# Optimization experiments

Measured on AMD Instinct MI355X. Metric: run time of the kernel, lower is better.

## Reference

```python
import jax, jax.numpy as jnp
import numpy as np

B, C, LH, LW, HH, HW = 8, 64, 128, 128, 64, 64


def conv3x3(x, w, groups=1):
    # x: NCHW, w: OIHW, stride 1, padding 1 (matches nn.Conv2d(k=3, p=1, bias=False))
    return jax.lax.conv_general_dilated(
        x, w, window_strides=(1, 1), padding=((1, 1), (1, 1)),
        feature_group_count=groups,
        dimension_numbers=('NCHW', 'OIHW', 'NCHW'))


def grid_sample_bilinear(img, grid):
    # F.grid_sample(mode='bilinear', padding_mode='zeros', align_corners=True)
    # img: (N, Cc, H, W); grid: (N, Ho, Wo, 2) with (x, y) in [-1, 1]
    N, Cc, H, W = img.shape
    gx = (grid[..., 0] + 1.0) * 0.5 * (W - 1)
    gy = (grid[..., 1] + 1.0) * 0.5 * (H - 1)
    x0 = jnp.floor(gx)
    y0 = jnp.floor(gy)
    wx1 = gx - x0
    wy1 = gy - y0

    def tap(xi, yi, wgt):
        valid = (xi >= 0) & (xi <= W - 1) & (yi >= 0) & (yi <= H - 1)
        xc = jnp.clip(xi, 0, W - 1).astype(jnp.int32)
        yc = jnp.clip(yi, 0, H - 1).astype(jnp.int32)
        v = jax.vmap(lambda im, y, x: im[:, y, x])(img, yc, xc)  # (N, Cc, Ho, Wo)
        return v * (wgt * valid)[:, None]

    return (tap(x0, y0, (1 - wx1) * (1 - wy1))
            + tap(x0 + 1, y0, wx1 * (1 - wy1))
            + tap(x0, y0 + 1, (1 - wx1) * wy1)
            + tap(x0 + 1, y0 + 1, wx1 * wy1))


def flow_warp(inp, flow, out_h, out_w):
    # base grid in [-1,1] (align_corners=True convention), flow normalized by (out_w, out_h)
    hs = jnp.linspace(-1.0, 1.0, out_h)
    ws = jnp.linspace(-1.0, 1.0, out_w)
    base = jnp.stack(jnp.meshgrid(ws, hs, indexing='xy'), axis=-1)  # (Ho, Wo, 2) as (x, y)
    norm = jnp.array([out_w, out_h], dtype=inp.dtype)
    grid = base[None].astype(inp.dtype) + jnp.transpose(flow, (0, 2, 3, 1)) / norm
    return grid_sample_bilinear(inp, grid)


def setup_inputs() -> dict:
    key = jax.random.key(0)
    k1, k2, k3, k4, k5, k6 = jax.random.split(key, 6)
    return {
        'low_feature': jax.random.normal(k1, (B, C, LH, LW), dtype=jnp.float32),
        'high_feature': jax.random.normal(k2, (B, C, HH, HW), dtype=jnp.float32),
        'w_conv_l': jax.random.normal(k3, (C, 1, 3, 3), dtype=jnp.float32) * 0.1,   # depthwise
        'w_conv_h': jax.random.normal(k4, (C, 1, 3, 3), dtype=jnp.float32) * 0.1,   # depthwise
        'w_flow': jax.random.normal(k5, (4 * C, C, 3, 3), dtype=jnp.float32) * 0.05,
        'w_gate': jax.random.normal(k6, (1, 4, 3, 3), dtype=jnp.float32) * 0.1,
    }


def reference(low_feature, high_feature, w_conv_l, w_conv_h, w_flow, w_gate):
    lb, ln, lh, lw = low_feature.shape
    hb, hn, hh, hw = high_feature.shape
    l_feature = conv3x3(low_feature, w_conv_l, groups=ln)
    h_feature = conv3x3(high_feature, w_conv_h, groups=hn)
    # F.interpolate(mode='bilinear', align_corners=False) == jax.image.resize bilinear
    h_feature = jax.image.resize(h_feature, (hb, hn, lh, lw), method='bilinear')
    flow = conv3x3(l_feature + h_feature, w_flow)          # (B, 4C, lh, lw)
    part = 2 * ln
    flow_h, flow_l = flow[:, :part], flow[:, part:]
    high_r = high_feature.reshape(hb * hn, 1, hh, hw)
    fh = flow_h.reshape(lb * ln, 2, lh, lw)
    high_warp = flow_warp(high_r, fh, lh, lw).reshape(lb, ln, lh, lw)
    low_r = low_feature.reshape(lb * ln, 1, lh, lw)
    fl = flow_l.reshape(lb * ln, 2, lh, lw)
    low_warp = flow_warp(low_r, fl, lh, lw).reshape(lb, ln, lh, lw)
    gate_in = jnp.concatenate([
        h_feature.mean(axis=1, keepdims=True),
        l_feature.mean(axis=1, keepdims=True),
        h_feature.max(axis=1, keepdims=True),
        l_feature.max(axis=1, keepdims=True)], axis=1)     # (B, 4, lh, lw)
    gates = jax.nn.sigmoid(conv3x3(gate_in, w_gate))
    return high_warp * gates + low_warp * (1.0 - gates)
```

## Files before the change

### kernel.cpp

```cpp
#include <hip/hip_runtime.h>
#include <math.h>

#define BB 8
#define CC 64
#define LHH 128
#define LWW 128
#define HHH 64
#define HWW 64

typedef __attribute__((ext_vector_type(8))) short short8v;
typedef __attribute__((ext_vector_type(4))) float f32x4;

typedef struct __attribute__((packed, aligned(4))) {
  float x, y;
} f2u;

#define BTS 584
#define SROWB 16640
#define SIMGB (130 * SROWB)
#define KROWB 8448

__device__ __forceinline__ unsigned short f2bf(float f) {
  unsigned u = __float_as_uint(f);
  unsigned r = (u + 0x7fffu + ((u >> 16) & 1u)) >> 16;
  return (unsigned short)r;
}

__global__ __launch_bounds__(256) void dw_high_prep_kernel(
    const float* __restrict__ hf, const float* __restrict__ w,
    float* __restrict__ out, const float* __restrict__ wflow,
    unsigned short* __restrict__ bt) {
  if (blockIdx.x >= 8192) {
    int t = (blockIdx.x - 8192) * 256 + threadIdx.x;
    if (t >= 256 * BTS) return;
    int oc2 = t / BTS;
    int kd = t - oc2 * BTS;
    unsigned short v = 0;
    if (kd < 576) {
      int c = oc2 >> 2;
      int j = oc2 & 3;
      int orig = (j >> 1) * 128 + 2 * c + (j & 1);
      int dydx = kd >> 6;
      int ci = kd & 63;
      v = f2bf(wflow[(orig * 64 + ci) * 9 + dydx]);
    }
    bt[t] = v;
    return;
  }
  int t = blockIdx.x * 256 + threadIdx.x;
  int x = t & 63;
  int y = (t >> 6) & 63;
  int c = (t >> 12) & 63;
  int b = t >> 18;
  const float* img = hf + ((size_t)(b * CC + c)) * (HHH * HWW);
  const float* wc = w + c * 9;
  const int xm = max(x - 1, 0), xp = min(x + 1, 63);
  const int ym = max(y - 1, 0), yp = min(y + 1, 63);
  const float mL = x > 0 ? 1.f : 0.f, mR = x < 63 ? 1.f : 0.f;
  const float mT = y > 0 ? 1.f : 0.f, mB = y < 63 ? 1.f : 0.f;
  const bool xz = (x == 0);
  const int dxp = xp - xm;
  f2u p0 = *(const f2u*)(img + ym * 64 + xm);
  f2u p1 = *(const f2u*)(img + y * 64 + xm);
  f2u p2 = *(const f2u*)(img + yp * 64 + xm);
  float r0p = img[ym * 64 + xm + dxp];
  float r1p = img[y * 64 + xm + dxp];
  float r2p = img[yp * 64 + xm + dxp];
  float r0x = xz ? p0.x : p0.y;
  float r1x = xz ? p1.x : p1.y;
  float r2x = xz ? p2.x : p2.y;
  float t0 = (wc[0] * mL) * p0.x + wc[1] * r0x + (wc[2] * mR) * r0p;
  float t1 = (wc[3] * mL) * p1.x + wc[4] * r1x + (wc[5] * mR) * r1p;
  float t2 = (wc[6] * mL) * p2.x + wc[7] * r2x + (wc[8] * mR) * r2p;
  out[t] = mT * t0 + t1 + mB * t2;
}

__global__ __launch_bounds__(512, 4) void fuse_sum_stats_kernel(
    const float* __restrict__ low, const float* __restrict__ hsm,
    const float* __restrict__ wl, unsigned short* __restrict__ sump,
    float* __restrict__ gate_in) {
  __shared__ unsigned short sumS[128 * 64];
  __shared__ float sh[4][4][128];
  __shared__ float wS[576];

  const int bid = blockIdx.x;
  const int b = bid & 7;
  const int y = bid >> 3;
  const int tid = threadIdx.x;
  const int x = tid & 127;
  const int q = tid >> 7;
  char* sbase = (char*)sump + (size_t)b * SIMGB;

  wS[tid] = wl[tid];
  if (tid < 64) wS[512 + tid] = wl[512 + tid];

  {
    const short8v z = {0, 0, 0, 0, 0, 0, 0, 0};
    if (y == 0) {
      for (int i = tid; i < 2080; i += 512) {
        int row = (i < 1040) ? 0 : 129;
        int o = (i % 1040) * 16;
        *(short8v*)(sbase + (size_t)row * SROWB + o) = z;
      }
    }
    if (tid < 16) {
      int side = tid >> 3;
      int o = (tid & 7) * 16;
      *(short8v*)(sbase + (size_t)(y + 1) * SROWB + side * (129 * 128) + o) = z;
    }
  }
  __syncthreads();

  float sy = 0.5f * y - 0.25f;
  float sx = 0.5f * x - 0.25f;
  float y0f = floorf(sy), x0f = floorf(sx);
  float wy = sy - y0f, wx = sx - x0f;
  int iy0 = (int)y0f, ix0 = (int)x0f;
  int iy0c = max(0, min(HHH - 1, iy0));
  int iy1c = max(0, min(HHH - 1, iy0 + 1));
  float w00 = (1.f - wy) * (1.f - wx), w01 = (1.f - wy) * wx;
  float w10 = wy * (1.f - wx), w11 = wy * wx;
  const int hxb = min(max(ix0, 0), HWW - 2);
  const bool hs0 = (ix0 <= hxb);
  const bool hs1 = (ix0 + 1 <= hxb);

  const int xm = max(x - 1, 0), xp = min(x + 1, 127);
  const int ym = max(y - 1, 0), yp = min(y + 1, 127);
  const float mL = x > 0 ? 1.f : 0.f, mR = x < 127 ? 1.f : 0.f;
  const float mT = y > 0 ? 1.f : 0.f, mB = y < 127 ? 1.f : 0.f;
  const bool xz = (x == 0);

  const unsigned lco = (unsigned)((b * CC + q * 16) * 16384);
  const unsigned hco = (unsigned)((b * CC + q * 16) * 4096);
  const unsigned ro0 = (unsigned)(ym * 128 + xm);
  const unsigned ro1 = (unsigned)(y * 128 + xm);
  const unsigned ro2 = (unsigned)(yp * 128 + xm);
  const unsigned dxp = (unsigned)(xp - xm);
  const unsigned ho0 = (unsigned)(iy0c * 64 + hxb);
  const unsigned ho1 = (unsigned)(iy1c * 64 + hxb);

  float hmean = 0.f, lmean = 0.f;
  float hmax = -3.402823466e+38f, lmax = -3.402823466e+38f;

  unsigned short sv[16];
#pragma unroll 8
  for (int j = 0; j < 16; ++j) {
    const unsigned lo_ = lco + (unsigned)(j * 16384);
    const float* wc = &wS[(q * 16 + j) * 9];
    f2u p0 = *(const f2u*)(low + (lo_ + ro0));
    f2u p1 = *(const f2u*)(low + (lo_ + ro1));
    f2u p2 = *(const f2u*)(low + (lo_ + ro2));
    float r0p = low[lo_ + ro0 + dxp];
    float r1p = low[lo_ + ro1 + dxp];
    float r2p = low[lo_ + ro2 + dxp];
    const unsigned ho_ = hco + (unsigned)(j * 4096);
    f2u q0 = *(const f2u*)(hsm + (ho_ + ho0));
    f2u q1 = *(const f2u*)(hsm + (ho_ + ho1));

    float r0x = xz ? p0.x : p0.y;
    float r1x = xz ? p1.x : p1.y;
    float r2x = xz ? p2.x : p2.y;
    float t0 = (wc[0] * mL) * p0.x + wc[1] * r0x + (wc[2] * mR) * r0p;
    float t1 = (wc[3] * mL) * p1.x + wc[4] * r1x + (wc[5] * mR) * r1p;
    float t2 = (wc[6] * mL) * p2.x + wc[7] * r2x + (wc[8] * mR) * r2p;
    float l = mT * t0 + t1 + mB * t2;

    float h00 = hs0 ? q0.x : q0.y;
    float h01 = hs1 ? q0.x : q0.y;
    float h10 = hs0 ? q1.x : q1.y;
    float h11 = hs1 ? q1.x : q1.y;
    float h = w00 * h00 + w01 * h01 + w10 * h10 + w11 * h11;

    sv[j] = f2bf(l + h);
    hmean += h;
    lmean += l;
    hmax = fmaxf(hmax, h);
    lmax = fmaxf(lmax, l);
  }

  {
    unsigned int pk[8];
#pragma unroll
    for (int j = 0; j < 8; ++j)
      pk[j] = (unsigned)sv[2 * j] | ((unsigned)sv[2 * j + 1] << 16);
    const int u0 = (x * 128 + q * 32) ^ ((x & 7) << 4);
    const int u1 = (x * 128 + q * 32 + 16) ^ ((x & 7) << 4);
    *(short8v*)((char*)sumS + u0) = *(short8v*)&pk[0];
    *(short8v*)((char*)sumS + u1) = *(short8v*)&pk[4];
  }
  sh[0][q][x] = hmean;
  sh[1][q][x] = lmean;
  sh[2][q][x] = hmax;
  sh[3][q][x] = lmax;
  __syncthreads();

  {
    char* dst = sbase + (size_t)(y + 1) * SROWB + 128;
#pragma unroll
    for (int pass = 0; pass < 2; ++pass) {
      int o = (tid + pass * 512) * 16;
      int L = o ^ (((o >> 7) & 7) << 4);
      *(short8v*)(dst + o) = *(const short8v*)((const char*)sumS + L);
    }
  }
  {
    const int s = q;
    float v0 = sh[s][0][x], v1 = sh[s][1][x], v2 = sh[s][2][x],
          v3 = sh[s][3][x];
    float r;
    if (s < 2)
      r = (v0 + v1 + v2 + v3) * (1.0f / CC);
    else
      r = fmaxf(fmaxf(v0, v1), fmaxf(v2, v3));
    gate_in[((size_t)(b * 4 + s)) * 16384 + y * 128 + x] = r;
  }
}

struct BSamp {
  f2u p0, p1;
  float mx0, mx1, my0, my1;
  bool s0, s1;
};

__device__ __forceinline__ BSamp bprep(const float* __restrict__ base,
                                       unsigned coff, int H, int W, float gx,
                                       float gy) {
  BSamp s;
  float x0f = floorf(gx), y0f = floorf(gy);
  float wx1 = gx - x0f, wy1 = gy - y0f;
  int x0 = (int)x0f, y0 = (int)y0f;
  int y1 = y0 + 1;
  s.mx0 = ((unsigned)x0 < (unsigned)W) ? 1.f - wx1 : 0.f;
  s.mx1 = ((unsigned)(x0 + 1) < (unsigned)W) ? wx1 : 0.f;
  s.my0 = ((unsigned)y0 < (unsigned)H) ? 1.f - wy1 : 0.f;
  s.my1 = ((unsigned)y1 < (unsigned)H) ? wy1 : 0.f;
  int xb = min(max(x0, 0), W - 2);
  int y0c = min(max(y0, 0), H - 1);
  int y1c = min(max(y1, 0), H - 1);
  s.p0 = *(const f2u*)(base + (coff + (unsigned)(y0c * W + xb)));
  s.p1 = *(const f2u*)(base + (coff + (unsigned)(y1c * W + xb)));
  s.s0 = (x0 <= xb);
  s.s1 = (x0 + 1 <= xb);
  return s;
}

__device__ __forceinline__ float bfin(const BSamp& s) {
  float v00 = s.s0 ? s.p0.x : s.p0.y;
  float v01 = s.s1 ? s.p0.x : s.p0.y;
  float v10 = s.s0 ? s.p1.x : s.p1.y;
  float v11 = s.s1 ? s.p1.x : s.p1.y;
  return s.my0 * (s.mx0 * v00 + s.mx1 * v01) +
         s.my1 * (s.mx0 * v10 + s.mx1 * v11);
}

__global__ __launch_bounds__(512, 4) void flow_gemm_combine_kernel(
    const unsigned short* __restrict__ sump,
    const unsigned short* __restrict__ bt, const float* __restrict__ low,
    const float* __restrict__ high, const float* __restrict__ gate_in,
    const float* __restrict__ wg, float* __restrict__ out) {
  __shared__ unsigned short ldsU[3 * 4224];
  __shared__ float gateS[64];

  const int bid = blockIdx.x;
  const int b = bid & 7;
  const int y = (bid >> 3) & 127;
  const int xh = bid >> 10;
  const int tid = threadIdx.x;
  const int lane = tid & 63;
  const int wid = tid >> 6;
  const int lr = lane & 15;
  const int lg = lane >> 4;

  {
    const char* src =
        (const char*)sump + (size_t)b * SIMGB + (size_t)y * SROWB + xh * 8192;
    char* dstb = (char*)ldsU;
#pragma unroll
    for (int pass = 0; pass < 3; ++pass) {
      int i = tid + pass * 512;
      int seg = i / 528;
      int wo = (i - seg * 528) * 16;
      int o = seg * KROWB + wo;
      int L = o ^ (((o >> 7) & 7) << 4);
      *(short8v*)(dstb + L) = *(const short8v*)(src + seg * SROWB + wo);
    }
    if (tid < 48) {
      int i = tid + 1536;
      int seg = i / 528;
      int wo = (i - seg * 528) * 16;
      int o = seg * KROWB + wo;
      int L = o ^ (((o >> 7) & 7) << 4);
      *(short8v*)(dstb + L) = *(const short8v*)(src + seg * SROWB + wo);
    }
  }

  if (tid < 64) {
    const int x = xh * 64 + tid;
    const int xm = max(x - 1, 0), xp = min(x + 1, 127);
    const int ym = max(y - 1, 0), yp = min(y + 1, 127);
    const float mL = x > 0 ? 1.f : 0.f, mR = x < 127 ? 1.f : 0.f;
    const float mT = y > 0 ? 1.f : 0.f, mB = y < 127 ? 1.f : 0.f;
    const float* gi = gate_in + (size_t)b * 4 * 16384;
    float acc0 = 0.f;
#pragma unroll
    for (int ic = 0; ic < 4; ++ic) {
      const float* img = gi + ic * 16384;
      const float* wc = wg + ic * 9;
      const float* r0 = img + ym * 128;
      const float* r1 = img + y * 128;
      const float* r2 = img + yp * 128;
      float t0 = (wc[0] * mL) * r0[xm] + wc[1] * r0[x] + (wc[2] * mR) * r0[xp];
      float t1 = (wc[3] * mL) * r1[xm] + wc[4] * r1[x] + (wc[5] * mR) * r1[xp];
      float t2 = (wc[6] * mL) * r2[xm] + wc[7] * r2[x] + (wc[8] * mR) * r2[xp];
      acc0 += mT * t0 + t1 + mB * t2;
    }
    gateS[tid] = 1.0f / (1.0f + expf(-acc0));
  }
  __syncthreads();

  f32x4 acc[4][2];
#pragma unroll
  for (int i = 0; i < 4; ++i)
#pragma unroll
    for (int j = 0; j < 2; ++j) acc[i][j] = (f32x4){0.f, 0.f, 0.f, 0.f};

  const char* rc = (const char*)ldsU;
  const unsigned short* btw = bt + (size_t)(wid * 32 + lr) * BTS + lg * 8;
  for (int dydx = 0; dydx < 9; ++dydx) {
    const int dy = dydx / 3;
    const int dxl = dydx - dy * 3;
#pragma unroll
    for (int cc = 0; cc < 2; ++cc) {
      short8v af[4], bfr[2];
#pragma unroll
      for (int mf = 0; mf < 4; ++mf) {
        const int p = dy * 66 + dxl + mf * 16 + lr;
        const int fa = (p * 128 + cc * 64 + lg * 16) ^ ((p & 7) << 4);
        af[mf] = *(const short8v*)(rc + fa);
      }
#pragma unroll
      for (int nf = 0; nf < 2; ++nf)
        bfr[nf] = *(const short8v*)&btw[nf * 16 * BTS + dydx * 64 + cc * 32];
#pragma unroll
      for (int mf = 0; mf < 4; ++mf)
#pragma unroll
        for (int nf = 0; nf < 2; ++nf)
          acc[mf][nf] = __builtin_amdgcn_mfma_f32_16x16x32_bf16(
              bfr[nf], af[mf], acc[mf][nf], 0, 0, 0);
    }
  }

  const float* lowb = low + (size_t)b * CC * 16384;
  const float* highb = high + (size_t)b * CC * 4096;
  float* outb = out + (size_t)b * CC * 16384;
  const float by = -1.0f + y * (2.0f / 127.0f);
  const float gyh_b = (by + 1.0f) * 31.5f;
  const float gyl_b = (by + 1.0f) * 63.5f;
  const int xg0 = xh * 64;
  const int c0 = wid * 8 + lg;
  const int c1 = c0 + 4;

#pragma unroll
  for (int mf = 0; mf < 4; ++mf) {
    const int x = xg0 + mf * 16 + lr;
    const float g = gateS[mf * 16 + lr];
    const float bx = -1.0f + x * (2.0f / 127.0f);
    const float gxh_b = (bx + 1.0f) * 31.5f;
    const float gxl_b = (bx + 1.0f) * 63.5f;

    BSamp sh0 = bprep(highb, (unsigned)(c0 * 4096), HHH, HWW,
                      fmaf(acc[mf][0][0], 63.0f / 256.0f, gxh_b),
                      fmaf(acc[mf][0][1], 63.0f / 256.0f, gyh_b));
    BSamp sl0 = bprep(lowb, (unsigned)(c0 * 16384), LHH, LWW,
                      fmaf(acc[mf][0][2], 127.0f / 256.0f, gxl_b),
                      fmaf(acc[mf][0][3], 127.0f / 256.0f, gyl_b));
    BSamp sh1 = bprep(highb, (unsigned)(c1 * 4096), HHH, HWW,
                      fmaf(acc[mf][1][0], 63.0f / 256.0f, gxh_b),
                      fmaf(acc[mf][1][1], 63.0f / 256.0f, gyh_b));
    BSamp sl1 = bprep(lowb, (unsigned)(c1 * 16384), LHH, LWW,
                      fmaf(acc[mf][1][2], 127.0f / 256.0f, gxl_b),
                      fmaf(acc[mf][1][3], 127.0f / 256.0f, gyl_b));

    float h0 = bfin(sh0), l0 = bfin(sl0);
    outb[(unsigned)(c0 * 16384 + y * 128 + x)] = fmaf(g, h0 - l0, l0);
    float h1 = bfin(sh1), l1 = bfin(sl1);
    outb[(unsigned)(c1 * 16384 + y * 128 + x)] = fmaf(g, h1 - l1, l1);
  }
}

extern "C" void kernel_launch(void* const* d_in, const int* in_sizes, int n_in,
                              void* d_out, int out_size, void* d_ws,
                              size_t ws_size, hipStream_t stream) {
  const float* low = (const float*)d_in[0];
  const float* high = (const float*)d_in[1];
  const float* w_conv_l = (const float*)d_in[2];
  const float* w_conv_h = (const float*)d_in[3];
  const float* w_flow = (const float*)d_in[4];
  const float* w_gate = (const float*)d_in[5];
  float* out = (float*)d_out;
  char* ws = (char*)d_ws;

  const size_t OFF_HSMALL = 0;
  const size_t OFF_SUMP = 8388608;
  const size_t OFF_GATEIN = 25694208;
  const size_t OFF_BT = 28315648;

  float* h_small = (float*)(ws + OFF_HSMALL);
  unsigned short* sump = (unsigned short*)(ws + OFF_SUMP);
  float* gate_in = (float*)(ws + OFF_GATEIN);
  unsigned short* bt = (unsigned short*)(ws + OFF_BT);

  dw_high_prep_kernel<<<8192 + 584, 256, 0, stream>>>(high, w_conv_h, h_small,
                                                      w_flow, bt);
  fuse_sum_stats_kernel<<<1024, 512, 0, stream>>>(low, h_small, w_conv_l, sump,
                                                  gate_in);
  flow_gemm_combine_kernel<<<2048, 512, 0, stream>>>(sump, bt, low, high,
                                                     gate_in, w_gate, out);
}
```

Before: 112.2 us.

## Split flow GEMM into two halves and overlap gather loads with MFMA

The flow-GEMM in the combine kernel is split into two column halves. The bilinear-sample gathers for the first half are issued before the MFMA loop of the second half runs, so their global-load latency overlaps with matrix work. The launch-bounds occupancy hint drops from 4 to 3 blocks per CU to leave room for the extra live registers holding in-flight samples. This trades occupancy for instruction-level overlap, and the B fragments are now loaded twice.

Measured after the change: 115.4 us. 2.8% more time.

```diff
diff --git a/kernel.cpp b/kernel.cpp
--- a/kernel.cpp
+++ b/kernel.cpp
@@ -253,7 +253,7 @@
          s.my1 * (s.mx0 * v10 + s.mx1 * v11);
 }
 
-__global__ __launch_bounds__(512, 4) void flow_gemm_combine_kernel(
+__global__ __launch_bounds__(512, 3) void flow_gemm_combine_kernel(
     const unsigned short* __restrict__ sump,
     const unsigned short* __restrict__ bt, const float* __restrict__ low,
     const float* __restrict__ high, const float* __restrict__ gate_in,
@@ -318,38 +318,8 @@
   }
   __syncthreads();
 
-  f32x4 acc[4][2];
-#pragma unroll
-  for (int i = 0; i < 4; ++i)
-#pragma unroll
-    for (int j = 0; j < 2; ++j) acc[i][j] = (f32x4){0.f, 0.f, 0.f, 0.f};
-
   const char* rc = (const char*)ldsU;
   const unsigned short* btw = bt + (size_t)(wid * 32 + lr) * BTS + lg * 8;
-  for (int dydx = 0; dydx < 9; ++dydx) {
-    const int dy = dydx / 3;
-    const int dxl = dydx - dy * 3;
-#pragma unroll
-    for (int cc = 0; cc < 2; ++cc) {
-      short8v af[4], bfr[2];
-#pragma unroll
-      for (int mf = 0; mf < 4; ++mf) {
-        const int p = dy * 66 + dxl + mf * 16 + lr;
-        const int fa = (p * 128 + cc * 64 + lg * 16) ^ ((p & 7) << 4);
-        af[mf] = *(const short8v*)(rc + fa);
-      }
-#pragma unroll
-      for (int nf = 0; nf < 2; ++nf)
-        bfr[nf] = *(const short8v*)&btw[nf * 16 * BTS + dydx * 64 + cc * 32];
-#pragma unroll
-      for (int mf = 0; mf < 4; ++mf)
-#pragma unroll
-        for (int nf = 0; nf < 2; ++nf)
-          acc[mf][nf] = __builtin_amdgcn_mfma_f32_16x16x32_bf16(
-              bfr[nf], af[mf], acc[mf][nf], 0, 0, 0);
-    }
-  }
-
   const float* lowb = low + (size_t)b * CC * 16384;
   const float* highb = high + (size_t)b * CC * 4096;
   float* outb = out + (size_t)b * CC * 16384;
@@ -360,31 +330,148 @@
   const int c0 = wid * 8 + lg;
   const int c1 = c0 + 4;
 
+  f32x4 aA00 = {0.f, 0.f, 0.f, 0.f}, aA01 = {0.f, 0.f, 0.f, 0.f};
+  f32x4 aA10 = {0.f, 0.f, 0.f, 0.f}, aA11 = {0.f, 0.f, 0.f, 0.f};
+  for (int dydx = 0; dydx < 9; ++dydx) {
+    const int dy = dydx / 3;
+    const int dxl = dydx - dy * 3;
 #pragma unroll
-  for (int mf = 0; mf < 4; ++mf) {
-    const int x = xg0 + mf * 16 + lr;
-    const float g = gateS[mf * 16 + lr];
-    const float bx = -1.0f + x * (2.0f / 127.0f);
-    const float gxh_b = (bx + 1.0f) * 31.5f;
-    const float gxl_b = (bx + 1.0f) * 63.5f;
-
-    BSamp sh0 = bprep(highb, (unsigned)(c0 * 4096), HHH, HWW,
-                      fmaf(acc[mf][0][0], 63.0f / 256.0f, gxh_b),
-                      fmaf(acc[mf][0][1], 63.0f / 256.0f, gyh_b));
-    BSamp sl0 = bprep(lowb, (unsigned)(c0 * 16384), LHH, LWW,
-                      fmaf(acc[mf][0][2], 127.0f / 256.0f, gxl_b),
-                      fmaf(acc[mf][0][3], 127.0f / 256.0f, gyl_b));
-    BSamp sh1 = bprep(highb, (unsigned)(c1 * 4096), HHH, HWW,
-                      fmaf(acc[mf][1][0], 63.0f / 256.0f, gxh_b),
-                      fmaf(acc[mf][1][1], 63.0f / 256.0f, gyh_b));
-    BSamp sl1 = bprep(lowb, (unsigned)(c1 * 16384), LHH, LWW,
-                      fmaf(acc[mf][1][2], 127.0f / 256.0f, gxl_b),
-                      fmaf(acc[mf][1][3], 127.0f / 256.0f, gyl_b));
-
-    float h0 = bfin(sh0), l0 = bfin(sl0);
-    outb[(unsigned)(c0 * 16384 + y * 128 + x)] = fmaf(g, h0 - l0, l0);
-    float h1 = bfin(sh1), l1 = bfin(sl1);
-    outb[(unsigned)(c1 * 16384 + y * 128 + x)] = fmaf(g, h1 - l1, l1);
+    for (int cc = 0; cc < 2; ++cc) {
+      const int p0 = dy * 66 + dxl + lr;
+      const int p1 = p0 + 16;
+      short8v af0 = *(const short8v*)(rc + ((p0 * 128 + cc * 64 + lg * 16) ^
+                                            ((p0 & 7) << 4)));
+      short8v af1 = *(const short8v*)(rc + ((p1 * 128 + cc * 64 + lg * 16) ^
+                                            ((p1 & 7) << 4)));
+      short8v b0 = *(const short8v*)&btw[dydx * 64 + cc * 32];
+      short8v b1 = *(const short8v*)&btw[16 * BTS + dydx * 64 + cc * 32];
+      aA00 = __builtin_amdgcn_mfma_f32_16x16x32_bf16(b0, af0, aA00, 0, 0, 0);
+      aA01 = __builtin_amdgcn_mfma_f32_16x16x32_bf16(b1, af0, aA01, 0, 0, 0);
+      aA10 = __builtin_amdgcn_mfma_f32_16x16x32_bf16(b0, af1, aA10, 0, 0, 0);
+      aA11 = __builtin_amdgcn_mfma_f32_16x16x32_bf16(b1, af1, aA11, 0, 0, 0);
+    }
+  }
+
+  const int xA0 = xg0 + lr;
+  const int xA1 = xg0 + 16 + lr;
+  const float gA0 = gateS[lr];
+  const float gA1 = gateS[16 + lr];
+  const float gxhA0 = (1.0f + (-1.0f + xA0 * (2.0f / 127.0f))) * 31.5f;
+  const float gxlA0 = (1.0f + (-1.0f + xA0 * (2.0f / 127.0f))) * 63.5f;
+  const float gxhA1 = (1.0f + (-1.0f + xA1 * (2.0f / 127.0f))) * 31.5f;
+  const float gxlA1 = (1.0f + (-1.0f + xA1 * (2.0f / 127.0f))) * 63.5f;
+
+  BSamp A0h = bprep(highb, (unsigned)(c0 * 4096), HHH, HWW,
+                    fmaf(aA00[0], 63.0f / 256.0f, gxhA0),
+                    fmaf(aA00[1], 63.0f / 256.0f, gyh_b));
+  BSamp A0l = bprep(lowb, (unsigned)(c0 * 16384), LHH, LWW,
+                    fmaf(aA00[2], 127.0f / 256.0f, gxlA0),
+                    fmaf(aA00[3], 127.0f / 256.0f, gyl_b));
+  BSamp A0h1 = bprep(highb, (unsigned)(c1 * 4096), HHH, HWW,
+                     fmaf(aA01[0], 63.0f / 256.0f, gxhA0),
+                     fmaf(aA01[1], 63.0f / 256.0f, gyh_b));
+  BSamp A0l1 = bprep(lowb, (unsigned)(c1 * 16384), LHH, LWW,
+                     fmaf(aA01[2], 127.0f / 256.0f, gxlA0),
+                     fmaf(aA01[3], 127.0f / 256.0f, gyl_b));
+  BSamp A1h = bprep(highb, (unsigned)(c0 * 4096), HHH, HWW,
+                    fmaf(aA10[0], 63.0f / 256.0f, gxhA1),
+                    fmaf(aA10[1], 63.0f / 256.0f, gyh_b));
+  BSamp A1l = bprep(lowb, (unsigned)(c0 * 16384), LHH, LWW,
+                    fmaf(aA10[2], 127.0f / 256.0f, gxlA1),
+                    fmaf(aA10[3], 127.0f / 256.0f, gyl_b));
+  BSamp A1h1 = bprep(highb, (unsigned)(c1 * 4096), HHH, HWW,
+                     fmaf(aA11[0], 63.0f / 256.0f, gxhA1),
+                     fmaf(aA11[1], 63.0f / 256.0f, gyh_b));
+  BSamp A1l1 = bprep(lowb, (unsigned)(c1 * 16384), LHH, LWW,
+                     fmaf(aA11[2], 127.0f / 256.0f, gxlA1),
+                     fmaf(aA11[3], 127.0f / 256.0f, gyl_b));
+
+  f32x4 aB00 = {0.f, 0.f, 0.f, 0.f}, aB01 = {0.f, 0.f, 0.f, 0.f};
+  f32x4 aB10 = {0.f, 0.f, 0.f, 0.f}, aB11 = {0.f, 0.f, 0.f, 0.f};
+  for (int dydx = 0; dydx < 9; ++dydx) {
+    const int dy = dydx / 3;
+    const int dxl = dydx - dy * 3;
+#pragma unroll
+    for (int cc = 0; cc < 2; ++cc) {
+      const int p0 = dy * 66 + dxl + 32 + lr;
+      const int p1 = p0 + 16;
+      short8v af0 = *(const short8v*)(rc + ((p0 * 128 + cc * 64 + lg * 16) ^
+                                            ((p0 & 7) << 4)));
+      short8v af1 = *(const short8v*)(rc + ((p1 * 128 + cc * 64 + lg * 16) ^
+                                            ((p1 & 7) << 4)));
+      short8v b0 = *(const short8v*)&btw[dydx * 64 + cc * 32];
+      short8v b1 = *(const short8v*)&btw[16 * BTS + dydx * 64 + cc * 32];
+      aB00 = __builtin_amdgcn_mfma_f32_16x16x32_bf16(b0, af0, aB00, 0, 0, 0);
+      aB01 = __builtin_amdgcn_mfma_f32_16x16x32_bf16(b1, af0, aB01, 0, 0, 0);
+      aB10 = __builtin_amdgcn_mfma_f32_16x16x32_bf16(b0, af1, aB10, 0, 0, 0);
+      aB11 = __builtin_amdgcn_mfma_f32_16x16x32_bf16(b1, af1, aB11, 0, 0, 0);
+    }
+  }
+
+  {
+    float h, l;
+    h = bfin(A0h);
+    l = bfin(A0l);
+    outb[(unsigned)(c0 * 16384 + y * 128 + xA0)] = fmaf(gA0, h - l, l);
+    h = bfin(A0h1);
+    l = bfin(A0l1);
+    outb[(unsigned)(c1 * 16384 + y * 128 + xA0)] = fmaf(gA0, h - l, l);
+    h = bfin(A1h);
+    l = bfin(A1l);
+    outb[(unsigned)(c0 * 16384 + y * 128 + xA1)] = fmaf(gA1, h - l, l);
+    h = bfin(A1h1);
+    l = bfin(A1l1);
+    outb[(unsigned)(c1 * 16384 + y * 128 + xA1)] = fmaf(gA1, h - l, l);
+  }
+
+  const int xB0 = xg0 + 32 + lr;
+  const int xB1 = xg0 + 48 + lr;
+  const float gB0 = gateS[32 + lr];
+  const float gB1 = gateS[48 + lr];
+  const float gxhB0 = (1.0f + (-1.0f + xB0 * (2.0f / 127.0f))) * 31.5f;
+  const float gxlB0 = (1.0f + (-1.0f + xB0 * (2.0f / 127.0f))) * 63.5f;
+  const float gxhB1 = (1.0f + (-1.0f + xB1 * (2.0f / 127.0f))) * 31.5f;
+  const float gxlB1 = (1.0f + (-1.0f + xB1 * (2.0f / 127.0f))) * 63.5f;
+
+  BSamp B0h = bprep(highb, (unsigned)(c0 * 4096), HHH, HWW,
+                    fmaf(aB00[0], 63.0f / 256.0f, gxhB0),
+                    fmaf(aB00[1], 63.0f / 256.0f, gyh_b));
+  BSamp B0l = bprep(lowb, (unsigned)(c0 * 16384), LHH, LWW,
+                    fmaf(aB00[2], 127.0f / 256.0f, gxlB0),
+                    fmaf(aB00[3], 127.0f / 256.0f, gyl_b));
+  BSamp B0h1 = bprep(highb, (unsigned)(c1 * 4096), HHH, HWW,
+                     fmaf(aB01[0], 63.0f / 256.0f, gxhB0),
+                     fmaf(aB01[1], 63.0f / 256.0f, gyh_b));
+  BSamp B0l1 = bprep(lowb, (unsigned)(c1 * 16384), LHH, LWW,
+                     fmaf(aB01[2], 127.0f / 256.0f, gxlB0),
+                     fmaf(aB01[3], 127.0f / 256.0f, gyl_b));
+  BSamp B1h = bprep(highb, (unsigned)(c0 * 4096), HHH, HWW,
+                    fmaf(aB10[0], 63.0f / 256.0f, gxhB1),
+                    fmaf(aB10[1], 63.0f / 256.0f, gyh_b));
+  BSamp B1l = bprep(lowb, (unsigned)(c0 * 16384), LHH, LWW,
+                    fmaf(aB10[2], 127.0f / 256.0f, gxlB1),
+                    fmaf(aB10[3], 127.0f / 256.0f, gyl_b));
+  BSamp B1h1 = bprep(highb, (unsigned)(c1 * 4096), HHH, HWW,
+                     fmaf(aB11[0], 63.0f / 256.0f, gxhB1),
+                     fmaf(aB11[1], 63.0f / 256.0f, gyh_b));
+  BSamp B1l1 = bprep(lowb, (unsigned)(c1 * 16384), LHH, LWW,
+                     fmaf(aB11[2], 127.0f / 256.0f, gxlB1),
+                     fmaf(aB11[3], 127.0f / 256.0f, gyl_b));
+
+  {
+    float h, l;
+    h = bfin(B0h);
+    l = bfin(B0l);
+    outb[(unsigned)(c0 * 16384 + y * 128 + xB0)] = fmaf(gB0, h - l, l);
+    h = bfin(B0h1);
+    l = bfin(B0l1);
+    outb[(unsigned)(c1 * 16384 + y * 128 + xB0)] = fmaf(gB0, h - l, l);
+    h = bfin(B1h);
+    l = bfin(B1l);
+    outb[(unsigned)(c0 * 16384 + y * 128 + xB1)] = fmaf(gB1, h - l, l);
+    h = bfin(B1h1);
+    l = bfin(B1l1);
+    outb[(unsigned)(c1 * 16384 + y * 128 + xB1)] = fmaf(gB1, h - l, l);
   }
 }
 
```
